# Kernel tuning notes

Hardware: AMD Instinct MI355X
Metric: run time of the kernel (lower is better)

Reference implementation:

```python
import jax, jax.numpy as jnp
import numpy as np

B, G, S, L, F = 2, 1024, 64, 16, 8   # batch, attention windows, tokens/window, cells/token, in_features
ATT, RANK, HC = 128, 32, 32          # att_dim, factorization rank, n_head_channels
LF = L * F


def setup_inputs() -> dict:
    key = jax.random.key(0)
    ks = jax.random.split(key, 14)
    s = 0.05
    return {
        "x": jax.random.normal(ks[0], (B, G, S, L, F), jnp.float32),
        # rank-factorized Q projection: (L*F) -> att_dim
        "Wq_u": jax.random.normal(ks[1], (LF, RANK), jnp.float32) * s,
        "Wq_v": jax.random.normal(ks[2], (RANK, ATT), jnp.float32) * s,
        # rank-factorized KV projection: (L*F) -> 2*att_dim (bias=True in source)
        "Wkv_u": jax.random.normal(ks[3], (LF, RANK), jnp.float32) * s,
        "Wkv_v": jax.random.normal(ks[4], (RANK, 2 * ATT), jnp.float32) * s,
        "kv_b": jnp.zeros((2 * ATT,), jnp.float32),
        # rank-factorized out layer: att_dim -> (L*F)
        "Wo_u": jax.random.normal(ks[5], (ATT, RANK), jnp.float32) * s,
        "Wo_v": jax.random.normal(ks[6], (RANK, LF), jnp.float32) * s,
        # per-token-element residual gate (init 1e-7 as in source)
        "gamma": jnp.full((L, F), 1e-7, jnp.float32),
        # factorized MLP: (L*F) -> att_dim -> (L*F)
        "W1": jax.random.normal(ks[7], (LF, ATT), jnp.float32) * s,
        "b1": jnp.zeros((ATT,), jnp.float32),
        "W2": jax.random.normal(ks[8], (ATT, LF), jnp.float32) * s,
        "b2": jnp.zeros((LF,), jnp.float32),
        "gamma_mlp": jnp.full((), 1e-7, jnp.float32),
    }


def _ln(t):
    # layer norm over the token dims (L, F), no affine
    m = t.mean(axis=(-2, -1), keepdims=True)
    v = t.var(axis=(-2, -1), keepdims=True)
    return (t - m) * jax.lax.rsqrt(v + 1e-5)


def reference(x, Wq_u, Wq_v, Wkv_u, Wkv_v, kv_b, Wo_u, Wo_v, gamma, W1, b1, W2, b2, gamma_mlp):
    b, g, sfx, l, f = x.shape
    lf = l * f
    h = _ln(x).reshape(b, g, sfx, lf)                 # [b,g,s,LF]
    q = (h @ Wq_u) @ Wq_v                              # [b,g,s,ATT]
    kv = (h @ Wkv_u) @ Wkv_v + kv_b                    # [b,g,s,2*ATT]
    k, v = jnp.split(kv, 2, axis=-1)
    nh = q.shape[-1] // HC
    def heads(t):
        return t.reshape(b, g, sfx, nh, HC).transpose(0, 1, 3, 2, 4)  # [b,g,H,s,hc]
    qh, kh, vh = heads(q), heads(k), heads(v)
    scores = jnp.einsum('bghsc,bghtc->bghst', qh, kh) / np.float32(np.sqrt(HC))
    attn = jax.nn.softmax(scores, axis=-1)             # [b,g,H,s,s]
    o = jnp.einsum('bghst,bghtc->bghsc', attn, vh)
    o = o.transpose(0, 1, 3, 2, 4).reshape(b, g, sfx, nh * HC)
    upd = ((o @ Wo_u) @ Wo_v).reshape(b, g, sfx, l, f)
    x1 = x + gamma * upd                               # 'shift' update with gamma gate
    h2 = _ln(x1).reshape(b, g, sfx, lf)
    m = jax.nn.gelu(h2 @ W1 + b1) @ W2 + b2
    return x1 + gamma_mlp * m.reshape(b, g, sfx, l, f)
```

## Files before the change

kernel.cpp:

```cpp
#include <hip/hip_runtime.h>

#define NWIN 2048

#define QKVT8_OFF 0
#define OT8_OFF  20480
#define W1T_OFF  36864
#define W2T8_OFF 69632
#define CVEC_OFF 86016

typedef __attribute__((ext_vector_type(8))) __bf16 bf16x8;
typedef __attribute__((ext_vector_type(8))) short s16x8;
typedef __attribute__((ext_vector_type(4))) short s16x4;
typedef __attribute__((ext_vector_type(4))) float f32x4;

static __device__ inline short f2bf(float f) {
    __bf16 b = (__bf16)f;
    return __builtin_bit_cast(short, b);
}
static __device__ inline float bf2f(short h) {
    unsigned u = ((unsigned)(unsigned short)h) << 16;
    return __builtin_bit_cast(float, u);
}
static __device__ inline bf16x8 ldbf8(const short* p) {
    return __builtin_bit_cast(bf16x8, *(const s16x8*)p);
}
static __device__ inline unsigned char f2fp8(float v) {
    return (unsigned char)__builtin_amdgcn_cvt_pk_fp8_f32(v, v, 0u, false);
}
static __device__ inline long ld8(const void* p) {
    return *(const long*)p;
}

__global__ __launch_bounds__(256) void fam_pre(
    const float* __restrict__ Wq_u, const float* __restrict__ Wq_v,
    const float* __restrict__ Wkv_u, const float* __restrict__ Wkv_v,
    const float* __restrict__ kv_b, const float* __restrict__ Wo_u,
    const float* __restrict__ Wo_v, const float* __restrict__ W1,
    const float* __restrict__ W2, unsigned char* __restrict__ ws8)
{
    const int b = blockIdx.x, tid = threadIdx.x;
    float* cvec = (float*)(ws8 + CVEC_OFF);
    if (b < 16) {
        __shared__ float Wv[4096];
        __shared__ float Wu[4096];
        __shared__ float N[4096];
        for (int i = tid; i < 4096; i += 256) {
            int r = i >> 7, c = i & 127;
            Wv[i] = Wkv_v[r*256 + 128 + c];
            Wu[i] = Wo_u[i];
        }
        __syncthreads();
        for (int i = tid; i < 4096; i += 256) {
            int h = i >> 10, u = (i >> 5) & 31, r = i & 31;
            float acc = 0.f;
            for (int c = 0; c < 32; ++c) acc += Wv[r*128 + h*32 + c] * Wu[(h*32 + c)*32 + u];
            N[i] = acc;
        }
        __syncthreads();
        for (int i = tid; i < 1024; i += 256) {
            int jj = i >> 7, hr = i & 127;
            int j = b*8 + jj, h = hr >> 5, r = hr & 31;
            float acc = 0.f;
            for (int u = 0; u < 32; ++u) acc += N[h*1024 + u*32 + r] * Wo_v[u*128 + j];
            ws8[OT8_OFF + j*128 + hr] = f2fp8(acc * 128.f);
        }
    } else if (b < 32) {
        short* w1t = (short*)(ws8 + W1T_OFF);
        int i0 = (b - 16) * 8;
        for (int t = tid; t < 1024; t += 256) {
            int ii = t >> 7, k = t & 127, i = i0 + ii;
            w1t[i*128 + k] = f2bf(W1[k*128 + i]);
        }
    } else if (b < 48) {
        int j0 = (b - 32) * 8;
        for (int t = tid; t < 1024; t += 256) {
            int jj = t >> 7, k = t & 127, j = j0 + jj;
            ws8[W2T8_OFF + j*128 + k] = f2fp8(W2[k*128 + j] * 16.f);
        }
    } else {
        const int sl = b - 48;
        __shared__ float Msh[4096];
        __shared__ float ov[32];
        const float sc = 0.17677669529663687f;
        for (int i = tid; i < 4096; i += 256) {
            int h = i >> 10, u = (i >> 5) & 31, r = i & 31;
            float acc = 0.f;
            for (int c = 0; c < 32; ++c)
                acc += Wq_v[u*128 + h*32 + c] * Wkv_v[r*256 + h*32 + c];
            Msh[i] = acc * sc;
        }
        __syncthreads();
        for (int i = tid; i < 2048; i += 256) {
            int c = sl*16 + (i >> 7), k = i & 127;
            int h = c >> 5, r = c & 31;
            float acc = 0.f;
            for (int u = 0; u < 32; ++u) acc += Wq_u[k*32 + u] * Msh[h*1024 + u*32 + r];
            ws8[QKVT8_OFF + c*128 + k] = f2fp8(acc * 256.f);
        }
        for (int i = tid; i < 512; i += 256) {
            int u = sl*4 + (i >> 7), k = i & 127;
            ws8[QKVT8_OFF + (128 + u)*128 + k] = f2fp8(Wkv_u[k*32 + u] * 16.f);
        }
        if (sl == 0) {
            if (tid < 32) {
                float a = 0.f;
                for (int att = 0; att < 128; ++att) a += kv_b[128 + att] * Wo_u[att*32 + tid];
                ov[tid] = a;
            }
            __syncthreads();
            if (tid < 128) {
                float a = 0.f;
                for (int u = 0; u < 32; ++u) a += ov[u] * Wo_v[u*128 + tid];
                cvec[tid] = a;
            }
        }
    }
}

#define SRA 136
#define SHQ 40
#define SHB 72

#define SM_RA8   0
#define SM_KV8   8704
#define SM_KVT8  11264
#define SM_HB8   13568
#define SM_TOTAL 32000

__global__ __launch_bounds__(256, 5) void fam_main(
    const float* __restrict__ x, const unsigned char* __restrict__ ws8,
    const float* __restrict__ gamma, const float* __restrict__ b1,
    const float* __restrict__ b2, const float* __restrict__ gmlp_p,
    float* __restrict__ out)
{
    __shared__ __align__(16) unsigned char SM[SM_TOTAL];
    unsigned char* RA8  = SM + SM_RA8;
    unsigned char* KV8  = SM + SM_KV8;
    unsigned char* KVT8 = SM + SM_KVT8;

    const float* cvec = (const float*)(ws8 + CVEC_OFF);
    const int tid = threadIdx.x;
    const int l   = tid & 63;
    const int wv  = tid >> 6;
    const int l15 = l & 15;
    const int lg  = l >> 4;
    const size_t base = (size_t)blockIdx.x * 8192;
    const float* __restrict__ xw   = x + base;
    float* __restrict__       outw = out + base;
    const int n0 = wv * 32;

    {
        int s = tid >> 2, c = tid & 3;
        float4 xr1[8];
        float sum = 0.f, sq = 0.f;
        #pragma unroll
        for (int j = 0; j < 8; ++j) {
            xr1[j] = *(const float4*)&xw[s*128 + c*32 + j*4];
            sum += xr1[j].x + xr1[j].y + xr1[j].z + xr1[j].w;
            sq  += xr1[j].x*xr1[j].x + xr1[j].y*xr1[j].y + xr1[j].z*xr1[j].z + xr1[j].w*xr1[j].w;
        }
        sum += __shfl_xor(sum, 1); sq += __shfl_xor(sq, 1);
        sum += __shfl_xor(sum, 2); sq += __shfl_xor(sq, 2);
        float mean = sum * (1.f/128.f);
        float var  = sq * (1.f/128.f) - mean*mean;
        float rinv = rsqrtf(var + 1e-5f);
        #pragma unroll
        for (int j = 0; j < 8; ++j) {
            unsigned w = 0;
            w = __builtin_amdgcn_cvt_pk_fp8_f32((xr1[j].x - mean)*rinv, (xr1[j].y - mean)*rinv, w, false);
            w = __builtin_amdgcn_cvt_pk_fp8_f32((xr1[j].z - mean)*rinv, (xr1[j].w - mean)*rinv, w, true);
            *(unsigned*)&RA8[s*SRA + c*32 + j*4] = w;
        }
    }
    __syncthreads();

    {
        long bA[4], bB[4], bC[4];
        #pragma unroll
        for (int kb = 0; kb < 4; ++kb) {
            bA[kb] = ld8(ws8 + QKVT8_OFF + (wv*16 + l15)*128 + kb*32 + lg*8);
            bB[kb] = ld8(ws8 + QKVT8_OFF + ((wv + 4)*16 + l15)*128 + kb*32 + lg*8);
        }
        if (wv >= 2) {
            #pragma unroll
            for (int kb = 0; kb < 4; ++kb)
                bC[kb] = ld8(ws8 + QKVT8_OFF + ((6 + wv)*16 + l15)*128 + kb*32 + lg*8);
        }
        unsigned char* HBA = SM + SM_HB8 + (wv >> 1)*4608;
        unsigned char* HBB = SM + SM_HB8 + (2 + (wv >> 1))*4608;
        const int rr = (wv & 1)*16 + l15;
        #pragma unroll
        for (int m = 0; m < 4; ++m) {
            long a[4];
            #pragma unroll
            for (int kb = 0; kb < 4; ++kb)
                a[kb] = ld8(RA8 + (m*16 + l15)*SRA + kb*32 + lg*8);
            f32x4 accA = {0.f,0.f,0.f,0.f}, accB = {0.f,0.f,0.f,0.f};
            #pragma unroll
            for (int kb = 0; kb < 4; ++kb) {
                accA = __builtin_amdgcn_mfma_f32_16x16x32_fp8_fp8(a[kb], bA[kb], accA, 0, 0, 0);
                accB = __builtin_amdgcn_mfma_f32_16x16x32_fp8_fp8(a[kb], bB[kb], accB, 0, 0, 0);
            }
            #pragma unroll
            for (int j = 0; j < 4; ++j) {
                int row = (m*16 + lg*4 + j)*SHB;
                HBA[row + rr] = f2fp8(accA[j] * 0.25f);
                HBB[row + rr] = f2fp8(accB[j] * 0.25f);
            }
            if (wv >= 2) {
                f32x4 accC = {0.f,0.f,0.f,0.f};
                #pragma unroll
                for (int kb = 0; kb < 4; ++kb)
                    accC = __builtin_amdgcn_mfma_f32_16x16x32_fp8_fp8(a[kb], bC[kb], accC, 0, 0, 0);
                int u = (wv - 2)*16 + l15;
                #pragma unroll
                for (int j = 0; j < 4; ++j)
                    KV8[(m*16 + lg*4 + j)*SHQ + u] = f2fp8(accC[j] * 0.25f);
                unsigned w = 0;
                w = __builtin_amdgcn_cvt_pk_fp8_f32(accC[0]*0.25f, accC[1]*0.25f, w, false);
                w = __builtin_amdgcn_cvt_pk_fp8_f32(accC[2]*0.25f, accC[3]*0.25f, w, true);
                *(unsigned*)&KVT8[u*SHB + m*16 + lg*4] = w;
            }
        }
    }
    __syncthreads();

    {
        const int h = wv;
        unsigned char* HB8h = SM + SM_HB8 + h*4608;
        long av[4], bq[4];
        #pragma unroll
        for (int m = 0; m < 4; ++m) av[m] = ld8(KV8 + (m*16 + l15)*SHQ + lg*8);
        #pragma unroll
        for (int n = 0; n < 4; ++n) bq[n] = ld8(HB8h + (n*16 + l15)*SHB + lg*8);
        f32x4 cc[4][4];
        #pragma unroll
        for (int m = 0; m < 4; ++m)
            #pragma unroll
            for (int n = 0; n < 4; ++n) {
                f32x4 z = {0.f, 0.f, 0.f, 0.f};
                cc[m][n] = __builtin_amdgcn_mfma_f32_16x16x32_fp8_fp8(av[m], bq[n], z, 0, 0, 0);
            }
        #pragma unroll
        for (int n = 0; n < 4; ++n) {
            float e[4][4];
            float sm = 0.f;
            #pragma unroll
            for (int m = 0; m < 4; ++m)
                #pragma unroll
                for (int j = 0; j < 4; ++j) {
                    e[m][j] = __expf(fminf(cc[m][n][j] * 0.00390625f, 30.f));
                    sm += e[m][j];
                }
            sm += __shfl_xor(sm, 16);
            sm += __shfl_xor(sm, 32);
            float rs64 = __builtin_amdgcn_rcpf(sm) * 64.f;
            int srow = (n*16 + l15) * SHB;
            #pragma unroll
            for (int m = 0; m < 4; ++m) {
                unsigned w = 0;
                w = __builtin_amdgcn_cvt_pk_fp8_f32(e[m][0]*rs64, e[m][1]*rs64, w, false);
                w = __builtin_amdgcn_cvt_pk_fp8_f32(e[m][2]*rs64, e[m][3]*rs64, w, true);
                *(unsigned*)&HB8h[srow + m*16 + lg*4] = w;
            }
        }
        long a8[4][2], b8[2][2];
        #pragma unroll
        for (int m = 0; m < 4; ++m)
            #pragma unroll
            for (int kb = 0; kb < 2; ++kb)
                a8[m][kb] = ld8(HB8h + (m*16 + l15)*SHB + kb*32 + lg*8);
        #pragma unroll
        for (int nn = 0; nn < 2; ++nn)
            #pragma unroll
            for (int kb = 0; kb < 2; ++kb)
                b8[nn][kb] = ld8(KVT8 + (nn*16 + l15)*SHB + kb*32 + lg*8);
        #pragma unroll
        for (int m = 0; m < 4; ++m)
            #pragma unroll
            for (int nn = 0; nn < 2; ++nn) {
                f32x4 acc = {0.f,0.f,0.f,0.f};
                acc = __builtin_amdgcn_mfma_f32_16x16x32_fp8_fp8(a8[m][0], b8[nn][0], acc, 0, 0, 0);
                acc = __builtin_amdgcn_mfma_f32_16x16x32_fp8_fp8(a8[m][1], b8[nn][1], acc, 0, 0, 0);
                #pragma unroll
                for (int j = 0; j < 4; ++j)
                    RA8[(m*16 + lg*4 + j)*SRA + h*32 + nn*16 + l15] = f2fp8(acc[j] * 0.03125f);
            }
    }
    __syncthreads();

    float x1v[4][2][4];
    short* XB = (short*)(SM + SM_HB8);

    {
        float xr[4][2][4];
        #pragma unroll
        for (int m = 0; m < 4; ++m)
            #pragma unroll
            for (int nn = 0; nn < 2; ++nn)
                #pragma unroll
                for (int j = 0; j < 4; ++j)
                    xr[m][nn][j] = xw[(m*16 + lg*4 + j)*128 + n0 + nn*16 + l15];
        long bo[2][4];
        float cv[2], gm[2];
        #pragma unroll
        for (int nn = 0; nn < 2; ++nn) {
            int col = n0 + nn*16 + l15;
            #pragma unroll
            for (int kb = 0; kb < 4; ++kb)
                bo[nn][kb] = ld8(ws8 + OT8_OFF + col*128 + kb*32 + lg*8);
            cv[nn] = cvec[col];
            gm[nn] = gamma[col];
        }
        f32x4 acc[4][2];
        #pragma unroll
        for (int m = 0; m < 4; ++m)
            #pragma unroll
            for (int nn = 0; nn < 2; ++nn) acc[m][nn] = (f32x4){0.f,0.f,0.f,0.f};
        #pragma unroll
        for (int m = 0; m < 4; ++m) {
            long a[4];
            #pragma unroll
            for (int kb = 0; kb < 4; ++kb)
                a[kb] = ld8(RA8 + (m*16 + l15)*SRA + kb*32 + lg*8);
            #pragma unroll
            for (int kb = 0; kb < 4; ++kb)
                #pragma unroll
                for (int nn = 0; nn < 2; ++nn)
                    acc[m][nn] = __builtin_amdgcn_mfma_f32_16x16x32_fp8_fp8(a[kb], bo[nn][kb], acc[m][nn], 0, 0, 0);
        }
        #pragma unroll
        for (int m = 0; m < 4; ++m)
            #pragma unroll
            for (int nn = 0; nn < 2; ++nn)
                #pragma unroll
                for (int j = 0; j < 4; ++j) {
                    int row = m*16 + lg*4 + j;
                    float v = xr[m][nn][j] + gm[nn] * (acc[m][nn][j] * 9.765625e-4f + cv[nn]);
                    x1v[m][nn][j] = v;
                    XB[row*SRA + n0 + nn*16 + l15] = f2bf(v);
                }
    }
    __syncthreads();

    {
        int s = tid >> 2, c = tid & 3;
        float sum = 0.f, sq = 0.f;
        #pragma unroll
        for (int jj = 0; jj < 8; ++jj) {
            s16x4 hv = *(const s16x4*)&XB[s*SRA + c*32 + jj*4];
            #pragma unroll
            for (int e = 0; e < 4; ++e) {
                float f = bf2f(hv[e]);
                sum += f; sq += f*f;
            }
        }
        sum += __shfl_xor(sum, 1); sq += __shfl_xor(sq, 1);
        sum += __shfl_xor(sum, 2); sq += __shfl_xor(sq, 2);
        float mean = sum * (1.f/128.f);
        float var  = sq * (1.f/128.f) - mean*mean;
        float rinv = rsqrtf(var + 1e-5f);
        #pragma unroll
        for (int jj = 0; jj < 8; ++jj) {
            s16x4 hv = *(const s16x4*)&XB[s*SRA + c*32 + jj*4];
            s16x4 ov;
            #pragma unroll
            for (int e = 0; e < 4; ++e) ov[e] = f2bf((bf2f(hv[e]) - mean) * rinv);
            *(s16x4*)&XB[s*SRA + c*32 + jj*4] = ov;
        }
    }
    __syncthreads();

    {
        const short* W1t = (const short*)(ws8 + W1T_OFF);
        bf16x8 bw1[2][4];
        float bb1[2];
        #pragma unroll
        for (int nn = 0; nn < 2; ++nn) {
            #pragma unroll
            for (int k = 0; k < 4; ++k)
                bw1[nn][k] = ldbf8(&W1t[(n0 + nn*16 + l15)*128 + k*32 + lg*8]);
            bb1[nn] = b1[n0 + nn*16 + l15];
        }
        #pragma unroll
        for (int m = 0; m < 4; ++m) {
            bf16x8 a[4];
            #pragma unroll
            for (int k = 0; k < 4; ++k)
                a[k] = ldbf8(&XB[(m*16 + l15)*SRA + k*32 + lg*8]);
            #pragma unroll
            for (int nn = 0; nn < 2; ++nn) {
                f32x4 acc = {0.f,0.f,0.f,0.f};
                #pragma unroll
                for (int k = 0; k < 4; ++k)
                    acc = __builtin_amdgcn_mfma_f32_16x16x32_bf16(a[k], bw1[nn][k], acc, 0, 0, 0);
                #pragma unroll
                for (int j = 0; j < 4; ++j) {
                    float t = acc[j] + bb1[nn];
                    float w = -1.5957691216057308f * (t + 0.044715f*t*t*t);
                    float g = t * __builtin_amdgcn_rcpf(1.f + __expf(w));
                    RA8[(m*16 + lg*4 + j)*SRA + n0 + nn*16 + l15] = f2fp8(g * 8.f);
                }
            }
        }
    }
    __syncthreads();

    {
        const float gmv = gmlp_p[0];
        long bw[2][4];
        float bb[2];
        #pragma unroll
        for (int nn = 0; nn < 2; ++nn) {
            int col = n0 + nn*16 + l15;
            #pragma unroll
            for (int kb = 0; kb < 4; ++kb)
                bw[nn][kb] = ld8(ws8 + W2T8_OFF + col*128 + kb*32 + lg*8);
            bb[nn] = b2[col];
        }
        #pragma unroll
        for (int m = 0; m < 4; ++m) {
            long a[4];
            #pragma unroll
            for (int kb = 0; kb < 4; ++kb)
                a[kb] = ld8(RA8 + (m*16 + l15)*SRA + kb*32 + lg*8);
            #pragma unroll
            for (int nn = 0; nn < 2; ++nn) {
                f32x4 acc = {0.f,0.f,0.f,0.f};
                #pragma unroll
                for (int kb = 0; kb < 4; ++kb)
                    acc = __builtin_amdgcn_mfma_f32_16x16x32_fp8_fp8(a[kb], bw[nn][kb], acc, 0, 0, 0);
                #pragma unroll
                for (int j = 0; j < 4; ++j)
                    outw[(m*16 + lg*4 + j)*128 + n0 + nn*16 + l15] =
                        x1v[m][nn][j] + gmv * (acc[j] * 0.0078125f + bb[nn]);
            }
        }
    }
}

extern "C" void kernel_launch(void* const* d_in, const int* in_sizes, int n_in,
                              void* d_out, int out_size, void* d_ws, size_t ws_size,
                              hipStream_t stream) {
    const float* x     = (const float*)d_in[0];
    const float* Wq_u  = (const float*)d_in[1];
    const float* Wq_v  = (const float*)d_in[2];
    const float* Wkv_u = (const float*)d_in[3];
    const float* Wkv_v = (const float*)d_in[4];
    const float* kv_b  = (const float*)d_in[5];
    const float* Wo_u  = (const float*)d_in[6];
    const float* Wo_v  = (const float*)d_in[7];
    const float* gamma = (const float*)d_in[8];
    const float* W1    = (const float*)d_in[9];
    const float* b1    = (const float*)d_in[10];
    const float* W2    = (const float*)d_in[11];
    const float* b2    = (const float*)d_in[12];
    const float* gmlp  = (const float*)d_in[13];
    unsigned char* ws8 = (unsigned char*)d_ws;
    float* out = (float*)d_out;

    fam_pre<<<56, 256, 0, stream>>>(Wq_u, Wq_v, Wkv_u, Wkv_v, kv_b, Wo_u, Wo_v, W1, W2, ws8);
    fam_main<<<NWIN, 256, 0, stream>>>(x, ws8, gamma, b1, b2, gmlp, out);
}
```

Before: 93.31 us.

## Fold second layer-norm into W1 GEMM epilogue and drop x1 register copies

```diff
diff --git a/kernel.cpp b/kernel.cpp
--- a/kernel.cpp
+++ b/kernel.cpp
@@ -7,6 +7,7 @@
 #define W1T_OFF  36864
 #define W2T8_OFF 69632
 #define CVEC_OFF 86016
+#define CSW1_OFF 86528
 
 typedef __attribute__((ext_vector_type(8))) __bf16 bf16x8;
 typedef __attribute__((ext_vector_type(8))) short s16x8;
@@ -40,6 +41,7 @@
 {
     const int b = blockIdx.x, tid = threadIdx.x;
     float* cvec = (float*)(ws8 + CVEC_OFF);
+    float* csW1 = (float*)(ws8 + CSW1_OFF);
     if (b < 16) {
         __shared__ float Wv[4096];
         __shared__ float Wu[4096];
@@ -70,6 +72,11 @@
         for (int t = tid; t < 1024; t += 256) {
             int ii = t >> 7, k = t & 127, i = i0 + ii;
             w1t[i*128 + k] = f2bf(W1[k*128 + i]);
+        }
+        if (b == 16 && tid < 128) {
+            float a = 0.f;
+            for (int k = 0; k < 128; ++k) a += W1[k*128 + tid];
+            csW1[tid] = a;
         }
     } else if (b < 48) {
         int j0 = (b - 32) * 8;
@@ -125,6 +132,7 @@
 #define SM_KV8   8704
 #define SM_KVT8  11264
 #define SM_HB8   13568
+#define SM_STATS (SM_HB8 + 17408)
 #define SM_TOTAL 32000
 
 __global__ __launch_bounds__(256, 5) void fam_main(
@@ -139,6 +147,7 @@
     unsigned char* KVT8 = SM + SM_KVT8;
 
     const float* cvec = (const float*)(ws8 + CVEC_OFF);
+    const float* csW1 = (const float*)(ws8 + CSW1_OFF);
     const int tid = threadIdx.x;
     const int l   = tid & 63;
     const int wv  = tid >> 6;
@@ -289,18 +298,10 @@
     }
     __syncthreads();
 
-    float x1v[4][2][4];
     short* XB = (short*)(SM + SM_HB8);
-
-    {
-        float xr[4][2][4];
-        #pragma unroll
-        for (int m = 0; m < 4; ++m)
-            #pragma unroll
-            for (int nn = 0; nn < 2; ++nn)
-                #pragma unroll
-                for (int j = 0; j < 4; ++j)
-                    xr[m][nn][j] = xw[(m*16 + lg*4 + j)*128 + n0 + nn*16 + l15];
+    float* stats = (float*)(SM + SM_STATS);
+
+    {
         long bo[2][4];
         float cv[2], gm[2];
         #pragma unroll
@@ -312,11 +313,6 @@
             cv[nn] = cvec[col];
             gm[nn] = gamma[col];
         }
-        f32x4 acc[4][2];
-        #pragma unroll
-        for (int m = 0; m < 4; ++m)
-            #pragma unroll
-            for (int nn = 0; nn < 2; ++nn) acc[m][nn] = (f32x4){0.f,0.f,0.f,0.f};
         #pragma unroll
         for (int m = 0; m < 4; ++m) {
             long a[4];
@@ -324,22 +320,21 @@
             for (int kb = 0; kb < 4; ++kb)
                 a[kb] = ld8(RA8 + (m*16 + l15)*SRA + kb*32 + lg*8);
             #pragma unroll
-            for (int kb = 0; kb < 4; ++kb)
-                #pragma unroll
-                for (int nn = 0; nn < 2; ++nn)
-                    acc[m][nn] = __builtin_amdgcn_mfma_f32_16x16x32_fp8_fp8(a[kb], bo[nn][kb], acc[m][nn], 0, 0, 0);
-        }
-        #pragma unroll
-        for (int m = 0; m < 4; ++m)
-            #pragma unroll
-            for (int nn = 0; nn < 2; ++nn)
+            for (int nn = 0; nn < 2; ++nn) {
+                f32x4 acc = {0.f,0.f,0.f,0.f};
+                #pragma unroll
+                for (int kb = 0; kb < 4; ++kb)
+                    acc = __builtin_amdgcn_mfma_f32_16x16x32_fp8_fp8(a[kb], bo[nn][kb], acc, 0, 0, 0);
+                int col = n0 + nn*16 + l15;
                 #pragma unroll
                 for (int j = 0; j < 4; ++j) {
                     int row = m*16 + lg*4 + j;
-                    float v = xr[m][nn][j] + gm[nn] * (acc[m][nn][j] * 9.765625e-4f + cv[nn]);
-                    x1v[m][nn][j] = v;
-                    XB[row*SRA + n0 + nn*16 + l15] = f2bf(v);
+                    float xv = xw[row*128 + col];
+                    float v = xv + gm[nn] * (acc[j] * 9.765625e-4f + cv[nn]);
+                    XB[row*SRA + col] = f2bf(v);
                 }
+            }
+        }
     }
     __syncthreads();
 
@@ -357,16 +352,11 @@
         }
         sum += __shfl_xor(sum, 1); sq += __shfl_xor(sq, 1);
         sum += __shfl_xor(sum, 2); sq += __shfl_xor(sq, 2);
-        float mean = sum * (1.f/128.f);
-        float var  = sq * (1.f/128.f) - mean*mean;
-        float rinv = rsqrtf(var + 1e-5f);
-        #pragma unroll
-        for (int jj = 0; jj < 8; ++jj) {
-            s16x4 hv = *(const s16x4*)&XB[s*SRA + c*32 + jj*4];
-            s16x4 ov;
-            #pragma unroll
-            for (int e = 0; e < 4; ++e) ov[e] = f2bf((bf2f(hv[e]) - mean) * rinv);
-            *(s16x4*)&XB[s*SRA + c*32 + jj*4] = ov;
+        if (c == 0) {
+            float mean = sum * (1.f/128.f);
+            float var  = sq * (1.f/128.f) - mean*mean;
+            stats[s*2]     = mean;
+            stats[s*2 + 1] = rsqrtf(var + 1e-5f);
         }
     }
     __syncthreads();
@@ -374,13 +364,15 @@
     {
         const short* W1t = (const short*)(ws8 + W1T_OFF);
         bf16x8 bw1[2][4];
-        float bb1[2];
+        float bb1[2], cw1[2];
         #pragma unroll
         for (int nn = 0; nn < 2; ++nn) {
+            int col = n0 + nn*16 + l15;
             #pragma unroll
             for (int k = 0; k < 4; ++k)
-                bw1[nn][k] = ldbf8(&W1t[(n0 + nn*16 + l15)*128 + k*32 + lg*8]);
-            bb1[nn] = b1[n0 + nn*16 + l15];
+                bw1[nn][k] = ldbf8(&W1t[col*128 + k*32 + lg*8]);
+            bb1[nn] = b1[col];
+            cw1[nn] = csW1[col];
         }
         #pragma unroll
         for (int m = 0; m < 4; ++m) {
@@ -388,6 +380,10 @@
             #pragma unroll
             for (int k = 0; k < 4; ++k)
                 a[k] = ldbf8(&XB[(m*16 + l15)*SRA + k*32 + lg*8]);
+            float2 st[4];
+            #pragma unroll
+            for (int j = 0; j < 4; ++j)
+                st[j] = *(const float2*)&stats[(m*16 + lg*4 + j)*2];
             #pragma unroll
             for (int nn = 0; nn < 2; ++nn) {
                 f32x4 acc = {0.f,0.f,0.f,0.f};
@@ -396,7 +392,8 @@
                     acc = __builtin_amdgcn_mfma_f32_16x16x32_bf16(a[k], bw1[nn][k], acc, 0, 0, 0);
                 #pragma unroll
                 for (int j = 0; j < 4; ++j) {
-                    float t = acc[j] + bb1[nn];
+                    float rinv = st[j].y, mean = st[j].x;
+                    float t = rinv*acc[j] - rinv*mean*cw1[nn] + bb1[nn];
                     float w = -1.5957691216057308f * (t + 0.044715f*t*t*t);
                     float g = t * __builtin_amdgcn_rcpf(1.f + __expf(w));
                     RA8[(m*16 + lg*4 + j)*SRA + n0 + nn*16 + l15] = f2fp8(g * 8.f);
@@ -430,10 +427,13 @@
                 #pragma unroll
                 for (int kb = 0; kb < 4; ++kb)
                     acc = __builtin_amdgcn_mfma_f32_16x16x32_fp8_fp8(a[kb], bw[nn][kb], acc, 0, 0, 0);
-                #pragma unroll
-                for (int j = 0; j < 4; ++j)
-                    outw[(m*16 + lg*4 + j)*128 + n0 + nn*16 + l15] =
-                        x1v[m][nn][j] + gmv * (acc[j] * 0.0078125f + bb[nn]);
+                int col = n0 + nn*16 + l15;
+                #pragma unroll
+                for (int j = 0; j < 4; ++j) {
+                    int row = m*16 + lg*4 + j;
+                    float x1f = bf2f(XB[row*SRA + col]);
+                    outw[row*128 + col] = x1f + gmv * (acc[j] * 0.0078125f + bb[nn]);
+                }
             }
         }
     }
```

New measurement: 98.27 us. 1.05x slower.
